# Kernel optimization log

Hardware: AMD Instinct MI355X
Metric: run time of the kernel (lower is better)

The kernel has to match this reference:

```python
import jax, jax.numpy as jnp
import numpy as np

K = 3  # kernel_size
S = 1  # stride
P = 1  # padding


def setup_inputs() -> dict:
    key = jax.random.key(0)
    ks = jax.random.split(key, 5)
    B, C, H, W, O = 4, 64, 128, 128, 64
    x = jax.random.normal(ks[0], (B, C, H, W), jnp.float32)
    # offset conv params (module inits these to 0; use small random values so the
    # bilinear-gather path is actually exercised with non-integer offsets)
    w_off = jax.random.normal(ks[1], (2 * K * K, C, K, K), jnp.float32) * 0.01
    b_off = jax.random.normal(ks[2], (2 * K * K,), jnp.float32) * 0.01
    # deformable conv params (torchvision DeformConv2d has bias=True by default)
    w_dcn = jax.random.normal(ks[3], (O, C, K, K), jnp.float32) * (1.0 / np.sqrt(C * K * K))
    b_dcn = jax.random.normal(ks[4], (O,), jnp.float32) * 0.01
    return {"x": x, "w_off": w_off, "b_off": b_off, "w_dcn": w_dcn, "b_dcn": b_dcn}


def _conv(x, w, b):
    y = jax.lax.conv_general_dilated(
        x, w, window_strides=(S, S), padding=[(P, P), (P, P)],
        dimension_numbers=("NCHW", "OIHW", "NCHW"))
    return y + b[None, :, None, None]


def _deform_conv2d(x, offset, w_dcn, b_dcn):
    # x: [B,C,H,W]; offset: [B, 2*K*K, Ho, Wo] with (dy, dx) interleaved per
    # kernel tap (row-major kh*K+kw), matching torchvision deform_conv2d.
    B, C, H, W = x.shape
    Ho, Wo = offset.shape[2], offset.shape[3]
    K2 = K * K
    off = offset.reshape(B, K2, 2, Ho, Wo)
    oy, ox = off[:, :, 0], off[:, :, 1]  # [B,K2,Ho,Wo]

    kh = (jnp.arange(K2) // K).astype(jnp.float32)
    kw = (jnp.arange(K2) % K).astype(jnp.float32)
    base_y = (jnp.arange(Ho) * S - P).astype(jnp.float32)
    base_x = (jnp.arange(Wo) * S - P).astype(jnp.float32)
    # fractional sampling locations: p0 + p_k + offset
    py = base_y[None, None, :, None] + kh[None, :, None, None] + oy  # [B,K2,Ho,Wo]
    px = base_x[None, None, None, :] + kw[None, :, None, None] + ox

    y0f = jnp.floor(py); x0f = jnp.floor(px)
    dy = py - y0f; dx = px - x0f
    y0 = y0f.astype(jnp.int32); x0 = x0f.astype(jnp.int32)

    def gather(yi, xi):
        # implicit zero padding: mask out-of-range corners
        valid = (yi >= 0) & (yi < H) & (xi >= 0) & (xi < W)
        yc = jnp.clip(yi, 0, H - 1)
        xc = jnp.clip(xi, 0, W - 1)
        v = jax.vmap(lambda xb, yb, xib: xb[:, yb, xib])(x, yc, xc)  # [B,C,K2,Ho,Wo]
        return v * valid[:, None].astype(x.dtype)

    v00 = gather(y0, x0)
    v01 = gather(y0, x0 + 1)
    v10 = gather(y0 + 1, x0)
    v11 = gather(y0 + 1, x0 + 1)

    wy = dy[:, None]; wx = dx[:, None]  # [B,1,K2,Ho,Wo]
    sampled = (v00 * (1 - wy) * (1 - wx) + v01 * (1 - wy) * wx
               + v10 * wy * (1 - wx) + v11 * wy * wx)  # [B,C,K2,Ho,Wo]

    O = w_dcn.shape[0]
    out = jnp.einsum("bckij,ock->boij", sampled, w_dcn.reshape(O, C, K2))
    return out + b_dcn[None, :, None, None]


def reference(x, w_off, b_off, w_dcn, b_dcn):
    offset = _conv(x, w_off, b_off)          # [B, 2*K*K, Ho, Wo]
    return _deform_conv2d(x, offset, w_dcn, b_dcn)
```

## Files before the change

### kernel.cpp

```cpp
#include <hip/hip_runtime.h>
#include <hip/hip_fp16.h>

#define B_ 4
#define H_ 128
#define W_ 128
#define HW_ 16384

typedef _Float16 half8 __attribute__((ext_vector_type(8)));
typedef float floatx4 __attribute__((ext_vector_type(4)));


__global__ __launch_bounds__(256) void k_prep(
    const float* __restrict__ x, const float* __restrict__ w_dcn,
    const float* __restrict__ w_off, __half* __restrict__ x_h,
    __half* __restrict__ W2L, __half* __restrict__ W0L)
{
    int bid = blockIdx.x;
    int t = threadIdx.x;
    if (bid < 1024) {
        __shared__ float tile[64][65];
        int base = bid * 64;
        int b = base >> 14;
        int pin = base & (HW_-1);
        #pragma unroll
        for (int it = 0; it < 16; ++it) {
            int c = it*4 + (t >> 6);
            int p = t & 63;
            tile[c][p] = x[b*(64*HW_) + c*HW_ + pin + p];
        }
        __syncthreads();
        #pragma unroll
        for (int it = 0; it < 8; ++it) {
            int p  = it*8 + (t >> 5);
            int c2 = (t & 31) * 2;
            __half2 h2 = __floats2half2_rn(tile[c2][p], tile[c2+1][p]);
            *(__half2*)(x_h + (size_t)(base + p)*64 + c2) = h2;
        }
    } else {
        int idx = (bid - 1024)*256 + t;
        if (idx < 36864) {
            int e = idx & 7, lane = (idx>>3) & 63, og = (idx>>9) & 3;
            int ks = (idx>>11) & 1, tap = idx >> 12;
            int o = og*16 + (lane & 15);
            int c = ks*32 + (lane >> 4)*8 + e;
            W2L[idx] = __float2half(w_dcn[o*576 + c*9 + tap]);
        } else {
            int i2 = idx - 36864;
            int e = i2 & 7, lane = (i2>>3) & 63, h = (i2>>9) & 1;
            int ks = (i2>>10) & 1, tap = i2 >> 11;
            int oc = h*16 + (lane & 15);
            int c = ks*32 + (lane >> 4)*8 + e;
            W0L[i2] = (oc < 18) ? __float2half(w_off[oc*576 + c*9 + tap])
                                : __float2half(0.f);
        }
    }
}

#define CHS2 3488
#define DESC_OFF 27904
#define SMEM_SZ 37120

__global__ __launch_bounds__(256, 4) void k_fused(
    const __half* __restrict__ x_hg, const _Float16* __restrict__ W2L,
    const _Float16* __restrict__ W0L, const float* __restrict__ b_off,
    const float* __restrict__ b_dcn, float* __restrict__ out)
{
    __shared__ __attribute__((aligned(16))) char smem[SMEM_SZ];
    char*     halo_c = smem;
    float*    offL   = (float*)(smem + DESC_OFF);
    char*     desc   = smem + DESC_OFF;

    int t = threadIdx.x;
    int lane = t & 63;
    int w = __builtin_amdgcn_readfirstlane(t >> 6);
    int m = lane & 15, q = lane >> 4;

    int bid  = blockIdx.x;
    int xcd  = bid & 7, sidx = bid >> 3;
    int orig = xcd*128 + sidx;
    int b    = orig >> 8;
    int rem  = orig & 255;
    int i0   = (rem >> 2) * 2;
    int j0   = (rem & 3) * 32;

    const _Float16* xb = (const _Float16*)x_hg + (size_t)b * (HW_*64);

    for (int idx = t; idx < 1728; idx += 256) {
        int ch = idx & 7, pl = idx >> 3;
        int hr = pl / 36, hx = pl - hr*36;
        int grow = min(max(i0 - 2 + hr, 0), H_-1);
        int gcol = min(max(j0 - 2 + hx, 0), W_-1);
        half8 v = *(const half8*)(xb + ((grow<<7) + gcol)*64 + ch*8);
        *(half8*)(halo_c + ch*CHS2 + pl*16) = v;
    }
    __syncthreads();

    floatx4 accA[2];
    #pragma unroll
    for (int h = 0; h < 2; ++h) accA[h] = (floatx4){0.f,0.f,0.f,0.f};

    const half8 hz = {0,0,0,0,0,0,0,0};
    int pcol = w*16 + m;
    int rA = pcol >> 5, cA = pcol & 31;
    #pragma unroll
    for (int tap = 0; tap < 9; ++tap) {
        int kh = tap/3, kw = tap - (tap/3)*3;
        int ii = i0 + rA - 1 + kh;
        int jj = j0 + cA - 1 + kw;
        bool valid = (ii >= 0) && (ii < H_) && (jj >= 0) && (jj < W_);
        int pixA = (rA + 1 + kh)*36 + (cA + 1 + kw);
        half8 a0 = *(const half8*)(halo_c + q*CHS2     + pixA*16);
        half8 a1 = *(const half8*)(halo_c + (q+4)*CHS2 + pixA*16);
        a0 = valid ? a0 : hz;
        a1 = valid ? a1 : hz;
        #pragma unroll
        for (int ks = 0; ks < 2; ++ks) {
            half8 a = ks ? a1 : a0;
            #pragma unroll
            for (int h = 0; h < 2; ++h) {
                half8 bf = *(const half8*)(W0L + (((tap*2+ks)*2+h)<<9) + (lane<<3));
                accA[h] = __builtin_amdgcn_mfma_f32_16x16x32_f16(a, bf, accA[h], 0, 0, 0);
            }
        }
    }
    #pragma unroll
    for (int h = 0; h < 2; ++h) {
        int oc = h*16 + m;
        if (oc < 18) {
            float bo = b_off[oc];
            #pragma unroll
            for (int r = 0; r < 4; ++r)
                offL[(w*16 + q*4 + r)*20 + oc] = accA[h][r] + bo;
        }
    }
    __syncthreads();

    uint4 dreg[3];
    #pragma unroll
    for (int e = 0; e < 3; ++e) {
        int idx = e*256 + t;
        if (idx < 576) {
            int pos = idx / 9;
            int tap = idx - pos*9;
            int kh = tap/3, kw = tap - (tap/3)*3;
            int r = pos >> 5, c = pos & 31;
            float2 o2 = *(const float2*)(offL + pos*20 + 2*tap);
            float py = (float)(i0 + r - 1 + kh) + o2.x;
            float px = (float)(j0 + c - 1 + kw) + o2.y;
            float y0f = floorf(py), x0f = floorf(px);
            float dy = py - y0f, dx = px - x0f;
            int y0 = (int)y0f, x0i = (int)x0f;
            int y1 = y0 + 1,  x1 = x0i + 1;
            bool vy0 = (y0>=0)&(y0<H_),   vy1 = (y1>=0)&(y1<H_);
            bool vx0 = (x0i>=0)&(x0i<W_), vx1 = (x1>=0)&(x1<W_);
            int yc0 = min(max(y0,0),H_-1),  yc1 = min(max(y1,0),H_-1);
            int xc0 = min(max(x0i,0),W_-1), xc1 = min(max(x1,0),W_-1);
            float w00 = (1.f-dy)*(1.f-dx) * ((vy0&&vx0)?1.f:0.f);
            float w01 = (1.f-dy)*dx       * ((vy0&&vx1)?1.f:0.f);
            float w10 = dy*(1.f-dx)       * ((vy1&&vx0)?1.f:0.f);
            float w11 = dy*dx             * ((vy1&&vx1)?1.f:0.f);
            int hy0 = yc0 - (i0-2), hy1 = yc1 - (i0-2);
            int hx0 = xc0 - (j0-2), hx1 = xc1 - (j0-2);
            bool inh = (hy0>=0)&(hy0<6)&(hy1>=0)&(hy1<6)
                     & (hx0>=0)&(hx0<36)&(hx1>=0)&(hx1<36);
            unsigned a0,a1,a2,a3;
            if (inh) { a0 = hy0*36+hx0; a1 = hy0*36+hx1; a2 = hy1*36+hx0; a3 = hy1*36+hx1; }
            else     { a0 = ((yc0<<7)+xc0) | 0x8000u; a1 = (yc0<<7)+xc1;
                       a2 = (yc1<<7)+xc0;             a3 = (yc1<<7)+xc1; }
            __half2 hw0 = __floats2half2_rn(w00, w01);
            __half2 hw1 = __floats2half2_rn(w10, w11);
            dreg[e].x = a0 | (a1 << 16);
            dreg[e].y = a2 | (a3 << 16);
            dreg[e].z = *(unsigned*)&hw0;
            dreg[e].w = *(unsigned*)&hw1;
        }
    }
    __syncthreads();
    #pragma unroll
    for (int e = 0; e < 3; ++e) {
        int idx = e*256 + t;
        if (idx < 576) *(uint4*)(desc + idx*16) = dreg[e];
    }
    __syncthreads();

    floatx4 acc[4];
    #pragma unroll
    for (int og = 0; og < 4; ++og) acc[og] = (floatx4){0.f,0.f,0.f,0.f};

    const char* hq0 = halo_c + q*CHS2;
    const char* hq1 = halo_c + (q+4)*CHS2;
    const _Float16* xq0 = xb + q*8;
    const _Float16* xq1 = xb + 32 + q*8;
    int mypos = w*16 + m;

    #pragma unroll 3
    for (int tap = 0; tap < 9; ++tap) {
        uint4 d = *(const uint4*)(desc + (mypos*9 + tap)*16);
        unsigned p0i = d.x & 0x7fffu, p1i = d.x >> 16;
        unsigned p2i = d.y & 0xffffu, p3i = d.y >> 16;
        bool inh = (d.x & 0x8000u) == 0u;
        unsigned short b00 = (unsigned short)(d.z & 0xffffu);
        unsigned short b01 = (unsigned short)(d.z >> 16);
        unsigned short b10 = (unsigned short)(d.w & 0xffffu);
        unsigned short b11 = (unsigned short)(d.w >> 16);
        _Float16 h00 = *(_Float16*)&b00, h01 = *(_Float16*)&b01;
        _Float16 h10 = *(_Float16*)&b10, h11 = *(_Float16*)&b11;
        half8 W00 = {h00,h00,h00,h00,h00,h00,h00,h00};
        half8 W01 = {h01,h01,h01,h01,h01,h01,h01,h01};
        half8 W10 = {h10,h10,h10,h10,h10,h10,h10,h10};
        half8 W11 = {h11,h11,h11,h11,h11,h11,h11,h11};
        half8 v00a,v01a,v10a,v11a, v00b,v01b,v10b,v11b;
        if (inh) {
            v00a = *(const half8*)(hq0 + p0i*16);  v00b = *(const half8*)(hq1 + p0i*16);
            v01a = *(const half8*)(hq0 + p1i*16);  v01b = *(const half8*)(hq1 + p1i*16);
            v10a = *(const half8*)(hq0 + p2i*16);  v10b = *(const half8*)(hq1 + p2i*16);
            v11a = *(const half8*)(hq0 + p3i*16);  v11b = *(const half8*)(hq1 + p3i*16);
        } else {
            v00a = *(const half8*)(xq0 + p0i*64);  v00b = *(const half8*)(xq1 + p0i*64);
            v01a = *(const half8*)(xq0 + p1i*64);  v01b = *(const half8*)(xq1 + p1i*64);
            v10a = *(const half8*)(xq0 + p2i*64);  v10b = *(const half8*)(xq1 + p2i*64);
            v11a = *(const half8*)(xq0 + p3i*64);  v11b = *(const half8*)(xq1 + p3i*64);
        }
        half8 sk0 = v00a*W00 + v01a*W01 + v10a*W10 + v11a*W11;
        half8 sk1 = v00b*W00 + v01b*W01 + v10b*W10 + v11b*W11;
        #pragma unroll
        for (int og = 0; og < 4; ++og) {
            half8 bf0 = *(const half8*)(W2L + (((tap*2+0)*4+og)<<9) + (lane<<3));
            acc[og] = __builtin_amdgcn_mfma_f32_16x16x32_f16(sk0, bf0, acc[og], 0, 0, 0);
            half8 bf1 = *(const half8*)(W2L + (((tap*2+1)*4+og)<<9) + (lane<<3));
            acc[og] = __builtin_amdgcn_mfma_f32_16x16x32_f16(sk1, bf1, acc[og], 0, 0, 0);
        }
    }
    __syncthreads();

    float* E = (float*)smem;
    #pragma unroll
    for (int og = 0; og < 4; ++og) {
        #pragma unroll
        for (int r = 0; r < 4; ++r)
            E[(w*16 + q*4 + r)*66 + og*16 + m] = acc[og][r];
    }
    __syncthreads();
    int obase = (b*64)*HW_ + i0*W_ + j0;
    int orow = (lane >> 5)*W_ + (lane & 31);
    #pragma unroll
    for (int rep = 0; rep < 16; ++rep) {
        int o = rep*4 + w;
        out[obase + o*HW_ + orow] = E[lane*66 + o] + b_dcn[o];
    }
}

extern "C" void kernel_launch(void* const* d_in, const int* in_sizes, int n_in,
                              void* d_out, int out_size, void* d_ws, size_t ws_size,
                              hipStream_t stream) {
    const float* x     = (const float*)d_in[0];
    const float* w_off = (const float*)d_in[1];
    const float* b_off = (const float*)d_in[2];
    const float* w_dcn = (const float*)d_in[3];
    const float* b_dcn = (const float*)d_in[4];
    float* out = (float*)d_out;

    __half* x_h = (__half*)d_ws;
    __half* W2L = (__half*)((char*)d_ws + 8388608);
    __half* W0L = (__half*)((char*)d_ws + 8388608 + 73728);

    k_prep<<<1024 + 216, 256, 0, stream>>>(x, w_dcn, w_off, x_h, W2L, W0L);
    k_fused<<<1024, 256, 0, stream>>>(x_h, (const _Float16*)W2L,
                                      (const _Float16*)W0L, b_off, b_dcn, out);
}
```

Baseline: 105.2 us.

## Drop NHWC fp16 pre-conversion of x and read fp32 NCHW directly in fused kernel

Removes the prep pass that transposed x into an NHWC fp16 workspace copy. The fused kernel now loads its halo tile directly from the fp32 NCHW input, converting to fp16 while writing shared memory. Out-of-halo bilinear taps do strided per-channel fp32 gathers. This saves an 8 MB write plus re-read and part of the prep launch, but halo loads and fallback gathers become scalar strided accesses with less coalescing.

```diff
diff --git a/kernel.cpp b/kernel.cpp
--- a/kernel.cpp
+++ b/kernel.cpp
@@ -10,49 +10,25 @@
 typedef float floatx4 __attribute__((ext_vector_type(4)));
 
 
-__global__ __launch_bounds__(256) void k_prep(
-    const float* __restrict__ x, const float* __restrict__ w_dcn,
-    const float* __restrict__ w_off, __half* __restrict__ x_h,
+__global__ __launch_bounds__(256) void k_prep_w(
+    const float* __restrict__ w_dcn, const float* __restrict__ w_off,
     __half* __restrict__ W2L, __half* __restrict__ W0L)
 {
-    int bid = blockIdx.x;
-    int t = threadIdx.x;
-    if (bid < 1024) {
-        __shared__ float tile[64][65];
-        int base = bid * 64;
-        int b = base >> 14;
-        int pin = base & (HW_-1);
-        #pragma unroll
-        for (int it = 0; it < 16; ++it) {
-            int c = it*4 + (t >> 6);
-            int p = t & 63;
-            tile[c][p] = x[b*(64*HW_) + c*HW_ + pin + p];
-        }
-        __syncthreads();
-        #pragma unroll
-        for (int it = 0; it < 8; ++it) {
-            int p  = it*8 + (t >> 5);
-            int c2 = (t & 31) * 2;
-            __half2 h2 = __floats2half2_rn(tile[c2][p], tile[c2+1][p]);
-            *(__half2*)(x_h + (size_t)(base + p)*64 + c2) = h2;
-        }
+    int idx = blockIdx.x*256 + threadIdx.x;
+    if (idx < 36864) {
+        int e = idx & 7, lane = (idx>>3) & 63, og = (idx>>9) & 3;
+        int ks = (idx>>11) & 1, tap = idx >> 12;
+        int o = og*16 + (lane & 15);
+        int c = ks*32 + (lane >> 4)*8 + e;
+        W2L[idx] = __float2half(w_dcn[o*576 + c*9 + tap]);
     } else {
-        int idx = (bid - 1024)*256 + t;
-        if (idx < 36864) {
-            int e = idx & 7, lane = (idx>>3) & 63, og = (idx>>9) & 3;
-            int ks = (idx>>11) & 1, tap = idx >> 12;
-            int o = og*16 + (lane & 15);
-            int c = ks*32 + (lane >> 4)*8 + e;
-            W2L[idx] = __float2half(w_dcn[o*576 + c*9 + tap]);
-        } else {
-            int i2 = idx - 36864;
-            int e = i2 & 7, lane = (i2>>3) & 63, h = (i2>>9) & 1;
-            int ks = (i2>>10) & 1, tap = i2 >> 11;
-            int oc = h*16 + (lane & 15);
-            int c = ks*32 + (lane >> 4)*8 + e;
-            W0L[i2] = (oc < 18) ? __float2half(w_off[oc*576 + c*9 + tap])
-                                : __float2half(0.f);
-        }
+        int i2 = idx - 36864;
+        int e = i2 & 7, lane = (i2>>3) & 63, h = (i2>>9) & 1;
+        int ks = (i2>>10) & 1, tap = i2 >> 11;
+        int oc = h*16 + (lane & 15);
+        int c = ks*32 + (lane >> 4)*8 + e;
+        W0L[i2] = (oc < 18) ? __float2half(w_off[oc*576 + c*9 + tap])
+                            : __float2half(0.f);
     }
 }
 
@@ -61,7 +37,7 @@
 #define SMEM_SZ 37120
 
 __global__ __launch_bounds__(256, 4) void k_fused(
-    const __half* __restrict__ x_hg, const _Float16* __restrict__ W2L,
+    const float* __restrict__ x, const _Float16* __restrict__ W2L,
     const _Float16* __restrict__ W0L, const float* __restrict__ b_off,
     const float* __restrict__ b_dcn, float* __restrict__ out)
 {
@@ -83,15 +59,23 @@
     int i0   = (rem >> 2) * 2;
     int j0   = (rem & 3) * 32;
 
-    const _Float16* xb = (const _Float16*)x_hg + (size_t)b * (HW_*64);
-
-    for (int idx = t; idx < 1728; idx += 256) {
-        int ch = idx & 7, pl = idx >> 3;
-        int hr = pl / 36, hx = pl - hr*36;
-        int grow = min(max(i0 - 2 + hr, 0), H_-1);
-        int gcol = min(max(j0 - 2 + hx, 0), W_-1);
-        half8 v = *(const half8*)(xb + ((grow<<7) + gcol)*64 + ch*8);
-        *(half8*)(halo_c + ch*CHS2 + pl*16) = v;
+    const float* xf = x + (size_t)b * (64*HW_);
+
+    #pragma unroll
+    for (int rep = 0; rep < 7; ++rep) {
+        int idx = rep*256 + t;
+        if (idx < 1728) {
+            int ch = idx / 216, pl = idx - ch*216;
+            int hr = pl / 36, hx = pl - hr*36;
+            int grow = min(max(i0 - 2 + hr, 0), H_-1);
+            int gcol = min(max(j0 - 2 + hx, 0), W_-1);
+            int gpix = (grow<<7) + gcol;
+            const float* s = xf + ch*8*HW_ + gpix;
+            half8 v;
+            #pragma unroll
+            for (int e = 0; e < 8; ++e) v[e] = (_Float16)s[e*HW_];
+            *(half8*)(halo_c + ch*CHS2 + pl*16) = v;
+        }
     }
     __syncthreads();
 
@@ -189,8 +173,6 @@
 
     const char* hq0 = halo_c + q*CHS2;
     const char* hq1 = halo_c + (q+4)*CHS2;
-    const _Float16* xq0 = xb + q*8;
-    const _Float16* xq1 = xb + 32 + q*8;
     int mypos = w*16 + m;
 
     #pragma unroll 3
@@ -216,10 +198,17 @@
             v10a = *(const half8*)(hq0 + p2i*16);  v10b = *(const half8*)(hq1 + p2i*16);
             v11a = *(const half8*)(hq0 + p3i*16);  v11b = *(const half8*)(hq1 + p3i*16);
         } else {
-            v00a = *(const half8*)(xq0 + p0i*64);  v00b = *(const half8*)(xq1 + p0i*64);
-            v01a = *(const half8*)(xq0 + p1i*64);  v01b = *(const half8*)(xq1 + p1i*64);
-            v10a = *(const half8*)(xq0 + p2i*64);  v10b = *(const half8*)(xq1 + p2i*64);
-            v11a = *(const half8*)(xq0 + p3i*64);  v11b = *(const half8*)(xq1 + p3i*64);
+            #pragma unroll
+            for (int e = 0; e < 8; ++e) {
+                v00a[e] = (_Float16)xf[(q*8+e)*HW_ + (int)p0i];
+                v00b[e] = (_Float16)xf[((q+4)*8+e)*HW_ + (int)p0i];
+                v01a[e] = (_Float16)xf[(q*8+e)*HW_ + (int)p1i];
+                v01b[e] = (_Float16)xf[((q+4)*8+e)*HW_ + (int)p1i];
+                v10a[e] = (_Float16)xf[(q*8+e)*HW_ + (int)p2i];
+                v10b[e] = (_Float16)xf[((q+4)*8+e)*HW_ + (int)p2i];
+                v11a[e] = (_Float16)xf[(q*8+e)*HW_ + (int)p3i];
+                v11b[e] = (_Float16)xf[((q+4)*8+e)*HW_ + (int)p3i];
+            }
         }
         half8 sk0 = v00a*W00 + v01a*W01 + v10a*W10 + v11a*W11;
         half8 sk1 = v00b*W00 + v01b*W01 + v10b*W10 + v11b*W11;
@@ -260,11 +249,10 @@
     const float* b_dcn = (const float*)d_in[4];
     float* out = (float*)d_out;
 
-    __half* x_h = (__half*)d_ws;
-    __half* W2L = (__half*)((char*)d_ws + 8388608);
-    __half* W0L = (__half*)((char*)d_ws + 8388608 + 73728);
-
-    k_prep<<<1024 + 216, 256, 0, stream>>>(x, w_dcn, w_off, x_h, W2L, W0L);
-    k_fused<<<1024, 256, 0, stream>>>(x_h, (const _Float16*)W2L,
+    __half* W2L = (__half*)d_ws;
+    __half* W0L = (__half*)((char*)d_ws + 73728);
+
+    k_prep_w<<<216, 256, 0, stream>>>(w_dcn, w_off, W2L, W0L);
+    k_fused<<<1024, 256, 0, stream>>>(x, (const _Float16*)W2L,
                                       (const _Float16*)W0L, b_off, b_dcn, out);
 }
```

Result: faster. 96.95 us (-7.8%).
